# Performance work log

Measured on AMD Instinct MI355X. Metric: run time of the kernel, lower is better.

## Reference

```python
import jax, jax.numpy as jnp
import numpy as np

B, S, D, H = 8, 2048, 1024, 64

def setup_inputs() -> dict:
    key = jax.random.key(0)
    ks = jax.random.split(key, 7)
    scale = 0.02
    return {
        "x": jax.random.normal(ks[0], (B, S, D), dtype=jnp.float32),
        "Wq": jax.random.normal(ks[1], (D, H), dtype=jnp.float32) * scale,
        "bq": jax.random.normal(ks[2], (H,), dtype=jnp.float32) * scale,
        "Wk": jax.random.normal(ks[3], (D, H), dtype=jnp.float32) * scale,
        "bk": jax.random.normal(ks[4], (H,), dtype=jnp.float32) * scale,
        "Wv": jax.random.normal(ks[5], (D, H), dtype=jnp.float32) * scale,
        "bv": jax.random.normal(ks[6], (H,), dtype=jnp.float32) * scale,
    }

def reference(x, Wq, bq, Wk, bk, Wv, bv):
    # Single-head causal self-attention (dropout in eval mode -> identity).
    q = x @ Wq + bq            # [B,S,H]
    k = x @ Wk + bk            # [B,S,H]
    v = x @ Wv + bv            # [B,S,H]
    scores = jnp.einsum("bqh,bkh->bqk", q, k)  # [B,S,S]
    s = q.shape[1]
    causal = jnp.tril(jnp.ones((s, s), dtype=bool))
    # Original masks with -inf BEFORE scaling; -inf/scale == -inf, so equivalent.
    scores = jnp.where(causal, scores, -jnp.inf) / jnp.sqrt(jnp.float32(k.shape[-1]))
    attn = jax.nn.softmax(scores, axis=-1)
    return jnp.einsum("bqk,bkh->bqh", attn, v)
```

## Files before the change

### kernel.cpp

```cpp
#include <hip/hip_runtime.h>
#include <math.h>

#define BATCH 8
#define SEQ   2048
#define DIM   1024
#define HD    64
#define NROWS (BATCH * SEQ)
#define CHUNK 256
#define NCHUNK 8
#define QTILE 64
#define NQT   (SEQ / QTILE)
#define QSCALE 0.1803368801f

typedef __attribute__((ext_vector_type(8))) short bf16x8;
typedef __attribute__((ext_vector_type(4))) float f32x4;

__device__ __forceinline__ unsigned short f2bf(float f) {
    unsigned u = __float_as_uint(f);
    u = (u + 0x7FFFu + ((u >> 16) & 1u)) >> 16;
    return (unsigned short)u;
}
__device__ __forceinline__ unsigned short f2bf_hu(float f) {
    return (unsigned short)((__float_as_uint(f) + 0x8000u) >> 16);
}
__device__ __forceinline__ float fast_exp2(float x) {
#if __has_builtin(__builtin_amdgcn_exp2f)
    return __builtin_amdgcn_exp2f(x);
#else
    return exp2f(x);
#endif
}

__device__ __forceinline__ void gld_lds16(const void* g, void* l) {
    __builtin_amdgcn_global_load_lds(
        (const __attribute__((address_space(1))) void*)g,
        (__attribute__((address_space(3))) void*)l, 16, 0, 0);
}


__global__ __launch_bounds__(256)
void prep_w_kernel(const float* __restrict__ Wq, const float* __restrict__ Wk,
                   const float* __restrict__ Wv, unsigned short* __restrict__ Wt)
{
    const int mat = blockIdx.y;
    const float* __restrict__ W = (mat == 0) ? Wq : (mat == 1) ? Wk : Wv;
    const int k0 = blockIdx.x * 64;
    __shared__ float T[64][65];
    const int t = threadIdx.x;
    #pragma unroll
    for (int i = 0; i < 16; ++i) {
        const int idx = t + i * 256;
        T[idx >> 6][idx & 63] = W[(size_t)(k0 + (idx >> 6)) * HD + (idx & 63)];
    }
    __syncthreads();
    const int n = t >> 2;
    const int c = t & 3;
    union { unsigned short h[16]; uint4 v[2]; } buf;
    #pragma unroll
    for (int j = 0; j < 16; ++j) buf.h[j] = f2bf(T[c * 16 + j][n]);
    unsigned short* dst = Wt + ((size_t)mat * HD + n) * DIM + k0 + c * 16;
    *(uint4*)dst       = buf.v[0];
    *(uint4*)(dst + 8) = buf.v[1];
}

__global__ __launch_bounds__(384)
void qkv_mfma_kernel(const float* __restrict__ x,
                     const unsigned short* __restrict__ Wt,
                     const float* __restrict__ bq, const float* __restrict__ bk,
                     const float* __restrict__ bv,
                     unsigned short* __restrict__ Qg,
                     unsigned short* __restrict__ Kg,
                     unsigned short* __restrict__ Vtg)
{
    __shared__ unsigned short Xs[32][128];
    __shared__ unsigned short Ws[192][128];

    const int t    = threadIdx.x;
    const int lane = t & 63;
    const int w    = t >> 6;
    const int col  = lane & 15;
    const int quad = lane >> 4;
    const int rh   = w & 1;
    const int mat  = w >> 1;
    const int row0 = blockIdx.x * 32;

    const int r4   = lane >> 4;
    const int ch16 = lane & 15;

    f32x4 acc[4];
    #pragma unroll
    for (int i = 0; i < 4; ++i) acc[i] = (f32x4){0.f, 0.f, 0.f, 0.f};

    for (int k0 = 0; k0 < DIM; k0 += 128) {
        __syncthreads();
        #pragma unroll
        for (int ii = 0; ii < 8; ++ii) {
            const int rbase = w * 32 + ii * 4;
            const int r = rbase + r4;
            gld_lds16(&Wt[(size_t)r * DIM + k0 + (ch16 ^ (r & 15)) * 8], &Ws[rbase][0]);
        }
        if (t < 256) {
            const int xr  = t >> 3;
            const int xc0 = t & 7;
            #pragma unroll
            for (int h = 0; h < 2; ++h) {
                const int g = xc0 + h * 8;
                const float* xp = &x[(size_t)(row0 + xr) * DIM + k0 + g * 8];
                const float4 v0 = *(const float4*)xp;
                const float4 v1 = *(const float4*)(xp + 4);
                uint4 o;
                o.x = ((__float_as_uint(v0.x) + 0x8000u) >> 16) | ((__float_as_uint(v0.y) + 0x8000u) & 0xFFFF0000u);
                o.y = ((__float_as_uint(v0.z) + 0x8000u) >> 16) | ((__float_as_uint(v0.w) + 0x8000u) & 0xFFFF0000u);
                o.z = ((__float_as_uint(v1.x) + 0x8000u) >> 16) | ((__float_as_uint(v1.y) + 0x8000u) & 0xFFFF0000u);
                o.w = ((__float_as_uint(v1.z) + 0x8000u) >> 16) | ((__float_as_uint(v1.w) + 0x8000u) & 0xFFFF0000u);
                *(uint4*)&Xs[xr][(g ^ (xr & 15)) * 8] = o;
            }
        }
        __syncthreads();
        #pragma unroll
        for (int ks = 0; ks < 4; ++ks) {
            const int fswz = ((ks * 4 + quad) ^ col) * 8;
            const bf16x8 a = *(const bf16x8*)&Xs[rh * 16 + col][fswz];
            #pragma unroll
            for (int nt = 0; nt < 4; ++nt) {
                const bf16x8 b = *(const bf16x8*)&Ws[mat * 64 + nt * 16 + col][fswz];
                acc[nt] = __builtin_amdgcn_mfma_f32_16x16x32_bf16(a, b, acc[nt], 0, 0, 0);
            }
        }
    }

    const int b    = row0 / SEQ;
    const int s0   = (row0 % SEQ) + rh * 16 + quad * 4;
    const int grow = row0 + rh * 16 + quad * 4;
    const float* __restrict__ bias = (mat == 0) ? bq : (mat == 1) ? bk : bv;
    const float oscale = (mat == 0) ? QSCALE : 1.0f;
    #pragma unroll
    for (int nt = 0; nt < 4; ++nt) {
        const int nn = nt * 16 + col;
        const float bvv = bias[nn];
        if (mat < 2) {
            unsigned short* __restrict__ o = (mat == 0) ? Qg : Kg;
            #pragma unroll
            for (int r = 0; r < 4; ++r)
                o[(size_t)(grow + r) * HD + nn] = f2bf((acc[nt][r] + bvv) * oscale);
        } else {
            const unsigned lo = (unsigned)f2bf(acc[nt][0] + bvv) | ((unsigned)f2bf(acc[nt][1] + bvv) << 16);
            const unsigned hi = (unsigned)f2bf(acc[nt][2] + bvv) | ((unsigned)f2bf(acc[nt][3] + bvv) << 16);
            *(uint2*)&Vtg[((size_t)b * HD + nn) * SEQ + s0] = make_uint2(lo, hi);
        }
    }
}

__global__ __launch_bounds__(256)
void attn_part_kernel(const unsigned short* __restrict__ Qg,
                      const unsigned short* __restrict__ Kg,
                      const unsigned short* __restrict__ Vtg,
                      float* __restrict__ Opart,
                      float* __restrict__ Lsum)
{
    const int xb = blockIdx.x;
    const int c  = xb >> 8;
    const int b  = (xb >> 5) & 7;
    const int qt = xb & 31;
    if (qt < c * 4) return;

    __shared__ unsigned short Ks[64][64];
    __shared__ unsigned short Vs[64][64];
    __shared__ unsigned short Ps[4][16][76];

    const int t    = threadIdx.x;
    const int w    = t >> 6;
    const int lane = t & 63;
    const int col  = lane & 15;
    const int quad = lane >> 4;
    const int q0w  = qt * QTILE + w * 16;
    const size_t gq = (size_t)b * SEQ + q0w;

    const bf16x8 aq0 = *(const bf16x8*)&Qg[(gq + col) * HD + quad * 8];
    const bf16x8 aq1 = *(const bf16x8*)&Qg[(gq + col) * HD + 32 + quad * 8];

    f32x4 oacc[4];
    #pragma unroll
    for (int n = 0; n < 4; ++n) oacc[n] = (f32x4){0.f, 0.f, 0.f, 0.f};
    float lpart[4] = {0.f, 0.f, 0.f, 0.f};

    const int kbeg   = c * CHUNK;
    const int kend   = min((c + 1) * CHUNK, (qt + 1) * QTILE);
    const int ntiles = (kend - kbeg + 63) >> 6;

    const int r8 = lane >> 3, ch = lane & 7;
    const int swzr = (ch ^ r8) * 8;
    const unsigned short* kgb = Kg  + (size_t)b * SEQ * HD;
    const unsigned short* vgb = Vtg + (size_t)b * HD * SEQ;

    for (int it = 0; it < ntiles; ++it) {
        const int j0 = kbeg + it * 64;
        __syncthreads();
        #pragma unroll
        for (int ii = 0; ii < 2; ++ii) {
            const int rb = w * 16 + ii * 8;
            gld_lds16(&kgb[(size_t)(j0 + rb + r8) * HD + swzr], &Ks[rb][0]);
            gld_lds16(&vgb[(size_t)(rb + r8) * SEQ + j0 + swzr], &Vs[rb][0]);
        }
        __syncthreads();

        if (j0 <= q0w + 15) {
            f32x4 scv[4];
            #pragma unroll
            for (int nt = 0; nt < 4; ++nt) {
                const int sw0 = (quad ^ (col & 7)) * 8;
                const int sw1 = ((4 + quad) ^ (col & 7)) * 8;
                const bf16x8 bk0 = *(const bf16x8*)&Ks[nt * 16 + col][sw0];
                const bf16x8 bk1 = *(const bf16x8*)&Ks[nt * 16 + col][sw1];
                f32x4 s = __builtin_amdgcn_mfma_f32_16x16x32_bf16(aq0, bk0, (f32x4){0.f,0.f,0.f,0.f}, 0, 0, 0);
                s = __builtin_amdgcn_mfma_f32_16x16x32_bf16(aq1, bk1, s, 0, 0, 0);
                scv[nt] = s;
            }
            const bool needmask = (j0 + 63 > q0w);
            #pragma unroll
            for (int r = 0; r < 4; ++r) {
                const int row = q0w + quad * 4 + r;
                #pragma unroll
                for (int nt = 0; nt < 4; ++nt) {
                    float s = scv[nt][r];
                    if (needmask)
                        s = (j0 + nt * 16 + col <= row) ? s : -INFINITY;
                    const float p = fast_exp2(s);
                    lpart[r] += p;
                    Ps[w][quad * 4 + r][nt * 16 + col] = f2bf_hu(p);
                }
            }
            #pragma unroll
            for (int ks = 0; ks < 2; ++ks) {
                const bf16x8 ap = *(const bf16x8*)&Ps[w][col][ks * 32 + quad * 8];
                const int fswz = ((ks * 4 + quad) ^ (col & 7)) * 8;
                #pragma unroll
                for (int n = 0; n < 4; ++n) {
                    const bf16x8 bv2 = *(const bf16x8*)&Vs[n * 16 + col][fswz];
                    oacc[n] = __builtin_amdgcn_mfma_f32_16x16x32_bf16(ap, bv2, oacc[n], 0, 0, 0);
                }
            }
        }
    }

    #pragma unroll
    for (int r = 0; r < 4; ++r) {
        #pragma unroll
        for (int off = 1; off < 16; off <<= 1)
            lpart[r] += __shfl_xor(lpart[r], off, 64);
    }

    const int blk = (b * NQT + qt) * NCHUNK + c;
    float* Ob = Opart + (size_t)blk * (QTILE * HD);
    #pragma unroll
    for (int n = 0; n < 4; ++n)
        #pragma unroll
        for (int r = 0; r < 4; ++r)
            Ob[(w * 16 + quad * 4 + r) * HD + n * 16 + col] = oacc[n][r];
    if (col == 0) {
        float* lb = Lsum + (size_t)blk * QTILE;
        #pragma unroll
        for (int r = 0; r < 4; ++r)
            lb[w * 16 + quad * 4 + r] = lpart[r];
    }
}

__global__ __launch_bounds__(256)
void combine_kernel(const float* __restrict__ Opart,
                    const float* __restrict__ Lsum,
                    float* __restrict__ out)
{
    const int gid = blockIdx.x * 256 + threadIdx.x;
    const int i   = gid >> 6;
    const int d   = gid & 63;
    const int b   = i >> 11;
    const int s   = i & 2047;
    const int qt  = s >> 6;
    const int r64 = s & 63;
    const int nc  = (s >> 8) + 1;
    const int blk0 = (b * NQT + qt) * NCHUNK;

    float L = 0.f, acc = 0.f;
    for (int cc = 0; cc < nc; ++cc) {
        L   += Lsum[(size_t)(blk0 + cc) * QTILE + r64];
        acc += Opart[(size_t)(blk0 + cc) * (QTILE * HD) + r64 * HD + d];
    }
    out[(size_t)i * HD + d] = acc / L;
}

extern "C" void kernel_launch(void* const* d_in, const int* in_sizes, int n_in,
                              void* d_out, int out_size, void* d_ws, size_t ws_size,
                              hipStream_t stream) {
    const float* x  = (const float*)d_in[0];
    const float* Wq = (const float*)d_in[1];
    const float* bq = (const float*)d_in[2];
    const float* Wk = (const float*)d_in[3];
    const float* bk = (const float*)d_in[4];
    const float* Wv = (const float*)d_in[5];
    const float* bv = (const float*)d_in[6];
    float* out = (float*)d_out;

    unsigned short* Wt  = (unsigned short*)d_ws;
    unsigned short* Qg  = Wt + (size_t)3 * HD * DIM;
    unsigned short* Kg  = Qg + (size_t)NROWS * HD;
    unsigned short* Vtg = Kg + (size_t)NROWS * HD;
    float* Opart = (float*)(Vtg + (size_t)BATCH * HD * SEQ);
    float* Lsum  = Opart + (size_t)BATCH * NQT * NCHUNK * QTILE * HD;

    prep_w_kernel<<<dim3(16, 3), 256, 0, stream>>>(Wq, Wk, Wv, Wt);
    qkv_mfma_kernel<<<dim3(NROWS / 32), 384, 0, stream>>>(x, Wt, bq, bk, bv, Qg, Kg, Vtg);
    attn_part_kernel<<<dim3(NCHUNK * BATCH * NQT), 256, 0, stream>>>(Qg, Kg, Vtg, Opart, Lsum);
    combine_kernel<<<dim3(NROWS * HD / 256), 256, 0, stream>>>(Opart, Lsum, out);
}
```

Baseline: 148.8 us.

## Prefetch x into registers, compact attention grid, store partials in bf16, vectorize combine

The QKV projection kernel now loads the next x tile into registers while the current tile is computed, and issues the W LDS loads after the x stores. The attention grid launches only the 144 valid (qtile, chunk) pairs per batch instead of early-exiting the masked blocks. Partial outputs are written as bf16 rather than fp32, halving that traffic. The combine kernel reads four values per thread and writes float4. The bf16 partials lose some accuracy in the final output.

```diff
diff --git a/kernel.cpp b/kernel.cpp
--- a/kernel.cpp
+++ b/kernel.cpp
@@ -91,23 +91,26 @@
     #pragma unroll
     for (int i = 0; i < 4; ++i) acc[i] = (f32x4){0.f, 0.f, 0.f, 0.f};
 
-    for (int k0 = 0; k0 < DIM; k0 += 128) {
+    const int xr  = t >> 3;
+    const int xc0 = t & 7;
+    const float* __restrict__ xrow = &x[(size_t)(row0 + xr) * DIM];
+    float4 xv[4];
+    if (t < 256) {
+        xv[0] = *(const float4*)(xrow + xc0 * 8);
+        xv[1] = *(const float4*)(xrow + xc0 * 8 + 4);
+        xv[2] = *(const float4*)(xrow + (xc0 + 8) * 8);
+        xv[3] = *(const float4*)(xrow + (xc0 + 8) * 8 + 4);
+    }
+
+    for (int it = 0; it < 8; ++it) {
+        const int k0 = it * 128;
         __syncthreads();
-        #pragma unroll
-        for (int ii = 0; ii < 8; ++ii) {
-            const int rbase = w * 32 + ii * 4;
-            const int r = rbase + r4;
-            gld_lds16(&Wt[(size_t)r * DIM + k0 + (ch16 ^ (r & 15)) * 8], &Ws[rbase][0]);
-        }
         if (t < 256) {
-            const int xr  = t >> 3;
-            const int xc0 = t & 7;
             #pragma unroll
             for (int h = 0; h < 2; ++h) {
                 const int g = xc0 + h * 8;
-                const float* xp = &x[(size_t)(row0 + xr) * DIM + k0 + g * 8];
-                const float4 v0 = *(const float4*)xp;
-                const float4 v1 = *(const float4*)(xp + 4);
+                const float4 v0 = xv[h * 2];
+                const float4 v1 = xv[h * 2 + 1];
                 uint4 o;
                 o.x = ((__float_as_uint(v0.x) + 0x8000u) >> 16) | ((__float_as_uint(v0.y) + 0x8000u) & 0xFFFF0000u);
                 o.y = ((__float_as_uint(v0.z) + 0x8000u) >> 16) | ((__float_as_uint(v0.w) + 0x8000u) & 0xFFFF0000u);
@@ -116,7 +119,20 @@
                 *(uint4*)&Xs[xr][(g ^ (xr & 15)) * 8] = o;
             }
         }
+        #pragma unroll
+        for (int ii = 0; ii < 8; ++ii) {
+            const int rbase = w * 32 + ii * 4;
+            const int r = rbase + r4;
+            gld_lds16(&Wt[(size_t)r * DIM + k0 + (ch16 ^ (r & 15)) * 8], &Ws[rbase][0]);
+        }
         __syncthreads();
+        if (it < 7 && t < 256) {
+            const float* xp = xrow + k0 + 128;
+            xv[0] = *(const float4*)(xp + xc0 * 8);
+            xv[1] = *(const float4*)(xp + xc0 * 8 + 4);
+            xv[2] = *(const float4*)(xp + (xc0 + 8) * 8);
+            xv[3] = *(const float4*)(xp + (xc0 + 8) * 8 + 4);
+        }
         #pragma unroll
         for (int ks = 0; ks < 4; ++ks) {
             const int fswz = ((ks * 4 + quad) ^ col) * 8;
@@ -155,14 +171,13 @@
 void attn_part_kernel(const unsigned short* __restrict__ Qg,
                       const unsigned short* __restrict__ Kg,
                       const unsigned short* __restrict__ Vtg,
-                      float* __restrict__ Opart,
+                      unsigned short* __restrict__ Opart,
                       float* __restrict__ Lsum)
 {
-    const int xb = blockIdx.x;
-    const int c  = xb >> 8;
-    const int b  = (xb >> 5) & 7;
-    const int qt = xb & 31;
-    if (qt < c * 4) return;
+    const int b = blockIdx.x;
+    int y = blockIdx.y, c = 0;
+    while (y >= 32 - 4 * c) { y -= 32 - 4 * c; ++c; }
+    const int qt = y + 4 * c;
 
     __shared__ unsigned short Ks[64][64];
     __shared__ unsigned short Vs[64][64];
@@ -251,12 +266,12 @@
     }
 
     const int blk = (b * NQT + qt) * NCHUNK + c;
-    float* Ob = Opart + (size_t)blk * (QTILE * HD);
+    unsigned short* Ob = Opart + (size_t)blk * (QTILE * HD);
     #pragma unroll
     for (int n = 0; n < 4; ++n)
         #pragma unroll
         for (int r = 0; r < 4; ++r)
-            Ob[(w * 16 + quad * 4 + r) * HD + n * 16 + col] = oacc[n][r];
+            Ob[(w * 16 + quad * 4 + r) * HD + n * 16 + col] = f2bf(oacc[n][r]);
     if (col == 0) {
         float* lb = Lsum + (size_t)blk * QTILE;
         #pragma unroll
@@ -266,13 +281,13 @@
 }
 
 __global__ __launch_bounds__(256)
-void combine_kernel(const float* __restrict__ Opart,
+void combine_kernel(const unsigned short* __restrict__ Opart,
                     const float* __restrict__ Lsum,
                     float* __restrict__ out)
 {
     const int gid = blockIdx.x * 256 + threadIdx.x;
-    const int i   = gid >> 6;
-    const int d   = gid & 63;
+    const int i   = gid >> 4;
+    const int d4  = (gid & 15) * 4;
     const int b   = i >> 11;
     const int s   = i & 2047;
     const int qt  = s >> 6;
@@ -280,12 +295,19 @@
     const int nc  = (s >> 8) + 1;
     const int blk0 = (b * NQT + qt) * NCHUNK;
 
-    float L = 0.f, acc = 0.f;
+    float L = 0.f;
+    float a0 = 0.f, a1 = 0.f, a2 = 0.f, a3 = 0.f;
     for (int cc = 0; cc < nc; ++cc) {
-        L   += Lsum[(size_t)(blk0 + cc) * QTILE + r64];
-        acc += Opart[(size_t)(blk0 + cc) * (QTILE * HD) + r64 * HD + d];
-    }
-    out[(size_t)i * HD + d] = acc / L;
+        L += Lsum[(size_t)(blk0 + cc) * QTILE + r64];
+        const uint2 u = *(const uint2*)(Opart + (size_t)(blk0 + cc) * (QTILE * HD) + r64 * HD + d4);
+        a0 += __uint_as_float(u.x << 16);
+        a1 += __uint_as_float(u.x & 0xFFFF0000u);
+        a2 += __uint_as_float(u.y << 16);
+        a3 += __uint_as_float(u.y & 0xFFFF0000u);
+    }
+    const float rL = 1.0f / L;
+    float4 o; o.x = a0 * rL; o.y = a1 * rL; o.z = a2 * rL; o.w = a3 * rL;
+    *(float4*)&out[(size_t)i * HD + d4] = o;
 }
 
 extern "C" void kernel_launch(void* const* d_in, const int* in_sizes, int n_in,
@@ -300,15 +322,15 @@
     const float* bv = (const float*)d_in[6];
     float* out = (float*)d_out;
 
-    unsigned short* Wt  = (unsigned short*)d_ws;
-    unsigned short* Qg  = Wt + (size_t)3 * HD * DIM;
-    unsigned short* Kg  = Qg + (size_t)NROWS * HD;
-    unsigned short* Vtg = Kg + (size_t)NROWS * HD;
-    float* Opart = (float*)(Vtg + (size_t)BATCH * HD * SEQ);
-    float* Lsum  = Opart + (size_t)BATCH * NQT * NCHUNK * QTILE * HD;
+    unsigned short* Wt    = (unsigned short*)d_ws;
+    unsigned short* Qg    = Wt + (size_t)3 * HD * DIM;
+    unsigned short* Kg    = Qg + (size_t)NROWS * HD;
+    unsigned short* Vtg   = Kg + (size_t)NROWS * HD;
+    unsigned short* Opart = Vtg + (size_t)BATCH * HD * SEQ;
+    float* Lsum = (float*)(Opart + (size_t)BATCH * NQT * NCHUNK * QTILE * HD);
 
     prep_w_kernel<<<dim3(16, 3), 256, 0, stream>>>(Wq, Wk, Wv, Wt);
     qkv_mfma_kernel<<<dim3(NROWS / 32), 384, 0, stream>>>(x, Wt, bq, bk, bv, Qg, Kg, Vtg);
-    attn_part_kernel<<<dim3(NCHUNK * BATCH * NQT), 256, 0, stream>>>(Qg, Kg, Vtg, Opart, Lsum);
-    combine_kernel<<<dim3(NROWS * HD / 256), 256, 0, stream>>>(Opart, Lsum, out);
-}
+    attn_part_kernel<<<dim3(8, 144), 256, 0, stream>>>(Qg, Kg, Vtg, Opart, Lsum);
+    combine_kernel<<<dim3(NROWS * 16 / 256), 256, 0, stream>>>(Opart, Lsum, out);
+}
```

After: 144.5 us. 2.8% less time.
